# Performance work log

Hardware: AMD Instinct MI355X
Metric: run time of the kernel (lower is better)

## Reference

```python
import jax, jax.numpy as jnp
import numpy as np
from jax import lax

BS, CNT, W, P, E, K, L = 32, 128, 2048, 1024, 8, 25, 2


def setup_inputs() -> dict:
    key = jax.random.key(0)
    ks = jax.random.split(key, 12)
    s = lambda k, shape, scale: jax.random.normal(k, shape, dtype=jnp.float32) * scale
    return {
        "x": s(ks[0], (BS, CNT, W), 1.0),
        "conv_w": s(ks[1], (L, E, 1, K), 0.2),
        "conv_b": s(ks[2], (L, E), 0.02),
        "wq": s(ks[3], (L, P, W), 0.02),
        "bq": s(ks[4], (L, P), 0.02),
        "wk": s(ks[5], (L, P, W), 0.02),
        "bk": s(ks[6], (L, P), 0.02),
        "wv": s(ks[7], (L, P, W), 0.02),
        "bv": s(ks[8], (L, P), 0.02),
        "wo": s(ks[9], (L, W, P), 0.02),
        "bo": s(ks[10], (L, W), 0.02),
    }


def _moe(x, w, b):
    # x: [bs, cnt, W]; w: [E, 1, K]; b: [E]
    bs, cnt, d = x.shape
    xf = x.reshape(bs * cnt, 1, d)
    pad = K // 2
    y = lax.conv_general_dilated(
        xf, w, window_strides=(1,), padding=[(pad, pad)],
        dimension_numbers=("NCH", "OIH", "NCH"))  # [bs*cnt, E, W]
    y = y + b[None, :, None]
    return y.mean(axis=1).reshape(bs, cnt, d)


def _fe(x, wq, bq, wk, bk, wv, bv, wo, bo):
    # x: [bs, cnt, W]; projections to P, FFT-domain attention, back to W
    q = jnp.einsum("bcw,pw->bcp", x, wq) + bq
    k = jnp.einsum("bcw,pw->bcp", x, wk) + bk
    v = jnp.einsum("bcw,pw->bcp", x, wv) + bv
    q_fft = jnp.fft.fft(q, axis=-1)
    k_fft = jnp.fft.fft(k, axis=-1)
    v_fft = jnp.fft.fft(v, axis=-1)
    scale = jnp.sqrt(jnp.float32(P))
    weighted = (k_fft * jnp.conj(q_fft)) / scale * v_fft
    wv_real = jnp.fft.ifft(weighted, axis=-1).real.astype(x.dtype)
    return jnp.einsum("bcp,wp->bcw", wv_real, wo) + bo


def reference(x, conv_w, conv_b, wq, bq, wk, bk, wv, bv, wo, bo):
    for l in range(L):
        x = _moe(x, conv_w[l], conv_b[l])
        x = _fe(x, wq[l], bq[l], wk[l], bk[l], wv[l], bv[l], wo[l], bo[l])
    return x
```

## Files before the change

### kernel.cpp

```cpp
#include <hip/hip_runtime.h>
#include <hip/hip_bf16.h>

#define BSZ 32
#define CNTS 128
#define WD 2048
#define PD 1024
#define ED 8
#define KSZ 25
#define LN 2
#define MROWS (BSZ*CNTS)
#define QKVN (3*PD)
#define NWL (PD*WD)

typedef _Float16 f16;
typedef __attribute__((ext_vector_type(8))) _Float16 f16x8;
typedef __attribute__((ext_vector_type(4))) float f32x4;
typedef __attribute__((ext_vector_type(2))) float f32x2;

#define PI_F 3.14159265358979323846f
#define PAD(a) ((a) + ((a) >> 5))

__global__ __launch_bounds__(256) void cvt_layer(
    const float* __restrict__ wq, const float* __restrict__ wk,
    const float* __restrict__ wv, const float* __restrict__ wo,
    f16* __restrict__ wqkv16, f16* __restrict__ wo16)
{
    const int i = (blockIdx.x * 256 + threadIdx.x) * 4;
    const float* src;
    f16* dst;
    if (i < 3*NWL) {
        dst = wqkv16 + i;
        src = (i < NWL) ? wq + i : (i < 2*NWL) ? wk + (i - NWL) : wv + (i - 2*NWL);
    } else {
        dst = wo16 + (i - 3*NWL);
        src = wo + (i - 3*NWL);
    }
    const float4 v = *(const float4*)src;
    f16 o[4];
    o[0] = (f16)v.x; o[1] = (f16)v.y; o[2] = (f16)v.z; o[3] = (f16)v.w;
    *(ushort4*)dst = *(const ushort4*)o;
}

template<typename IT>
__global__ __launch_bounds__(256) void conv_moe(
    const IT* __restrict__ xin,
    const float* __restrict__ cw,
    const float* __restrict__ cb,
    f16* __restrict__ xo)
{
    __shared__ float srow[WD];
    __shared__ float swb[KSZ];
    __shared__ float sbb;
    const int tid = threadIdx.x;
    const size_t row = blockIdx.x;
    if (tid < KSZ) {
        float s = 0.f;
        for (int e = 0; e < ED; ++e) s += cw[e*KSZ + tid];
        swb[tid] = s * (1.f/ED);
    }
    if (tid == 32) {
        float s = 0.f;
        for (int e = 0; e < ED; ++e) s += cb[e];
        sbb = s * (1.f/ED);
    }
    const IT* xr = xin + row*WD;
    if constexpr (sizeof(IT) == 2) {
        const f16x8 v = *(const f16x8*)(xr + tid*8);
        #pragma unroll
        for (int j = 0; j < 8; ++j) srow[tid*8 + j] = (float)v[j];
    } else {
        const float4 v0 = *(const float4*)(xr + tid*8);
        const float4 v1 = *(const float4*)(xr + tid*8 + 4);
        srow[tid*8+0] = v0.x; srow[tid*8+1] = v0.y; srow[tid*8+2] = v0.z; srow[tid*8+3] = v0.w;
        srow[tid*8+4] = v1.x; srow[tid*8+5] = v1.y; srow[tid*8+6] = v1.z; srow[tid*8+7] = v1.w;
    }
    __syncthreads();
    const float bb = sbb;
    float w[32];
    #pragma unroll
    for (int k = 0; k < 32; ++k) {
        const int idx = tid*8 + k - (KSZ/2);
        w[k] = (idx >= 0 && idx < WD) ? srow[idx] : 0.f;
    }
    f16 o[8];
    #pragma unroll
    for (int j = 0; j < 8; ++j) {
        float acc = bb;
        #pragma unroll
        for (int k = 0; k < KSZ; ++k) acc = fmaf(w[j+k], swb[k], acc);
        o[j] = (f16)acc;
    }
    *(f16x8*)(xo + row*WD + tid*8) = *(const f16x8*)o;
}

template<typename OT>
__global__ __launch_bounds__(256, 2) void gemm_f16(
    const f16* __restrict__ A,
    const f16* __restrict__ B,
    const float* __restrict__ c0, const float* __restrict__ c1, const float* __restrict__ c2,
    OT* __restrict__ out,
    const int K, const int N)
{
    __shared__ f16 sA[128*64];
    __shared__ f16 sB[128*64];
    const int tid  = threadIdx.x;
    const int m0   = blockIdx.x * 128;
    const int n0   = blockIdx.y * 128;
    const int lane = tid & 63;
    const int wave = tid >> 6;
    const int wm   = (wave >> 1) * 64;
    const int wn   = (wave & 1) * 64;
    const int quad = lane >> 4;
    const int r16  = lane & 15;

    f32x4 acc[4][4] = {};

    int aoff[4];
    #pragma unroll
    for (int t = 0; t < 4; ++t) {
        const int s = tid + 256*t;
        const int row = s >> 3;
        const int sc8 = ((s & 7) ^ (row & 7)) * 8;
        aoff[t] = row * K + sc8;
    }

    int aBase[4], aXor[4], bBase[4], bXor[4];
    #pragma unroll
    for (int i = 0; i < 4; ++i) {
        const int ra = wm + i*16 + r16;
        aBase[i] = ra << 3; aXor[i] = ra & 7;
        const int rb = wn + i*16 + r16;
        bBase[i] = rb << 3; bXor[i] = rb & 7;
    }

    const size_t mK = (size_t)m0 * K;
    const size_t nK = (size_t)n0 * K;

    for (int kb = 0; kb < K; kb += 64) {
        #pragma unroll
        for (int t = 0; t < 4; ++t) {
            const int s = tid + 256*t;
            __builtin_amdgcn_global_load_lds(
                (const __attribute__((address_space(1))) unsigned int*)(A + mK + aoff[t] + kb),
                (__attribute__((address_space(3))) unsigned int*)&sA[s*8], 16, 0, 0);
            __builtin_amdgcn_global_load_lds(
                (const __attribute__((address_space(1))) unsigned int*)(B + nK + aoff[t] + kb),
                (__attribute__((address_space(3))) unsigned int*)&sB[s*8], 16, 0, 0);
        }
        __syncthreads();

        #pragma unroll
        for (int ks = 0; ks < 2; ++ks) {
            const int c = ks*4 + quad;
            f16x8 af[4], bfm[4];
            #pragma unroll
            for (int i = 0; i < 4; ++i)
                af[i] = *(const f16x8*)&sA[(aBase[i] | (c ^ aXor[i])) * 8];
            #pragma unroll
            for (int j = 0; j < 4; ++j)
                bfm[j] = *(const f16x8*)&sB[(bBase[j] | (c ^ bXor[j])) * 8];
            #pragma unroll
            for (int i = 0; i < 4; ++i)
                #pragma unroll
                for (int j = 0; j < 4; ++j)
                    acc[i][j] = __builtin_amdgcn_mfma_f32_16x16x32_f16(af[i], bfm[j], acc[i][j], 0, 0, 0);
        }
        __syncthreads();
    }

    #pragma unroll
    for (int j = 0; j < 4; ++j) {
        const int col = n0 + wn + j*16 + r16;
        const float bv = (col < 1024) ? c0[col] : (col < 2048) ? c1[col-1024] : c2[col-2048];
        #pragma unroll
        for (int i = 0; i < 4; ++i) {
            #pragma unroll
            for (int r = 0; r < 4; ++r) {
                const int rowg = m0 + wm + i*16 + quad*4 + r;
                out[(size_t)rowg*N + col] = (OT)(acc[i][j][r] + bv);
            }
        }
    }
}

__global__ __launch_bounds__(512, 2) void gemm192(
    const f16* __restrict__ A,
    const f16* __restrict__ B,
    const float* __restrict__ c0, const float* __restrict__ c1, const float* __restrict__ c2,
    f16* __restrict__ out,
    const int K, const int N)
{
    __shared__ __align__(16) f16 sA[2][2][128*64];
    __shared__ __align__(16) f16 sB[2][3][64*64];

    const int tid  = threadIdx.x;
    const int lane = tid & 63;
    const int wave = tid >> 6;
    const int wr   = wave >> 2;
    const int wc   = wave & 3;
    const int quad = lane >> 4;
    const int r16  = lane & 15;
    const int xrA  = r16 & 7;

    const int orig = blockIdx.x;
    const int xcd  = orig & 7;
    const int loc  = orig >> 3;
    const int mt   = (xcd >> 1) * 4 + (loc & 3);
    const int nt   = (xcd & 1) * 8 + (loc >> 2);
    const int m0   = mt * 256;
    const int n0   = nt * 192;

    f32x4 acc[8][3] = {};
    f16x8 bf[3][2];
    f16x8 aX0, aX1, aX2, aX3, aY0, aY1, aY2, aY3, aZ0, aZ1, aZ2, aZ3;

    int soffA[2];
    #pragma unroll
    for (int t = 0; t < 2; ++t) {
        const int s = tid + 512*t;
        const int row = s >> 3;
        soffA[t] = row * K + (((s & 7) ^ (row & 7)) * 8);
    }
    int soffB;
    {
        const int row = tid >> 3;
        soffB = row * K + (((tid & 7) ^ (row & 7)) * 8);
    }

    int bPiece[3], bBase[3], bXor[3];
    #pragma unroll
    for (int j = 0; j < 3; ++j) {
        const int rb = wc*48 + j*16 + r16;
        bPiece[j] = rb >> 6;
        bBase[j]  = (rb & 63) << 3;
        bXor[j]   = rb & 7;
    }

    const f16* Abase[2] = { A + (size_t)m0 * K, A + (size_t)(m0 + 128) * K };
    const f16* Bp[3]    = { B + (size_t)n0 * K, B + (size_t)(n0 + 64) * K,
                            B + (size_t)(n0 + 128) * K };

    #define STAGE_A(BUF, HALF, GOFF)                                              \
      { _Pragma("unroll") for (int t = 0; t < 2; ++t) {                           \
          __builtin_amdgcn_global_load_lds(                                       \
            (const __attribute__((address_space(1))) unsigned int*)(Abase[HALF] + soffA[t] + (GOFF)), \
            (__attribute__((address_space(3))) unsigned int*)&sA[BUF][HALF][(tid + 512*t)*8], \
            16, 0, 0); } }

    #define STAGE_B(BUF, PIECE, GOFF)                                             \
      { __builtin_amdgcn_global_load_lds(                                         \
          (const __attribute__((address_space(1))) unsigned int*)(Bp[PIECE] + soffB + (GOFF)), \
          (__attribute__((address_space(3))) unsigned int*)&sB[BUF][PIECE][tid*8], \
          16, 0, 0); }

    #define LDA(BUF, ROW, C) \
      (*(const f16x8*)&sA[BUF][wr][ (((ROW) << 3) + ((C) ^ xrA)) * 8 ])

    #define LDB(BUF, J, C) \
      (*(const f16x8*)&sB[BUF][bPiece[J]][ (bBase[J] + ((C) ^ bXor[J])) * 8 ])

    #define READ_BF(BUF)                                                          \
      { _Pragma("unroll") for (int j = 0; j < 3; ++j) {                           \
          bf[j][0] = LDB(BUF, j, quad);                                           \
          bf[j][1] = LDB(BUF, j, 4 + quad);                                       \
        } }

    #define READ_A(BUF, Q, D0, D1, D2, D3)                                        \
      D0 = LDA(BUF, (2*(Q))*16   + r16, quad);                                    \
      D1 = LDA(BUF, (2*(Q))*16   + r16, 4 + quad);                                \
      D2 = LDA(BUF, (2*(Q)+1)*16 + r16, quad);                                    \
      D3 = LDA(BUF, (2*(Q)+1)*16 + r16, 4 + quad);

    #define MFMA_Q(Q, D0, D1, D2, D3)                                             \
      __builtin_amdgcn_s_setprio(1);                                              \
      { _Pragma("unroll") for (int jj = 0; jj < 3; ++jj) {                        \
          acc[2*(Q)][jj]   = __builtin_amdgcn_mfma_f32_16x16x32_f16(D0, bf[jj][0], acc[2*(Q)][jj],   0,0,0); \
          acc[2*(Q)+1][jj] = __builtin_amdgcn_mfma_f32_16x16x32_f16(D2, bf[jj][0], acc[2*(Q)+1][jj], 0,0,0); \
        } }                                                                       \
      { _Pragma("unroll") for (int jj = 0; jj < 3; ++jj) {                        \
          acc[2*(Q)][jj]   = __builtin_amdgcn_mfma_f32_16x16x32_f16(D1, bf[jj][1], acc[2*(Q)][jj],   0,0,0); \
          acc[2*(Q)+1][jj] = __builtin_amdgcn_mfma_f32_16x16x32_f16(D3, bf[jj][1], acc[2*(Q)+1][jj], 0,0,0); \
        } }                                                                       \
      __builtin_amdgcn_s_setprio(0);

    #define LGKM(n) asm volatile("s_waitcnt lgkmcnt(" #n ")" ::: "memory");       \
                    __builtin_amdgcn_sched_barrier(0);
    #define VMC(n)  asm volatile("s_waitcnt vmcnt(" #n ")" ::: "memory");
    #define BAR()   __builtin_amdgcn_s_barrier();

    STAGE_B(0, 0, 0); STAGE_B(0, 1, 0); STAGE_B(0, 2, 0);
    STAGE_A(0, 0, 0); STAGE_A(0, 1, 0);
    STAGE_B(1, 0, 64); STAGE_B(1, 1, 64); STAGE_B(1, 2, 64);
    VMC(3)
    BAR()

    const int NIT = K >> 7;
    for (int it = 0; it < NIT; ++it) {
        const bool kl = (it == NIT - 1);
        const int kb1 = (2*it + 1) * 64;
        const int kb2 = kb1 + 64;
        const int kb3 = kb1 + 128;

        STAGE_A(1, 0, kb1);
        READ_BF(0)
        READ_A(0, 0, aX0, aX1, aX2, aX3)
        LGKM(0)
        MFMA_Q(0, aX0, aX1, aX2, aX3)
        BAR()
        STAGE_A(1, 1, kb1);
        READ_A(0, 1, aY0, aY1, aY2, aY3)
        READ_A(0, 2, aZ0, aZ1, aZ2, aZ3)
        LGKM(4)
        MFMA_Q(1, aY0, aY1, aY2, aY3)
        if (!kl) { STAGE_B(0, 0, kb2); STAGE_B(0, 1, kb2); }
        READ_A(0, 3, aX0, aX1, aX2, aX3)
        LGKM(4)
        MFMA_Q(2, aZ0, aZ1, aZ2, aZ3)
        if (!kl) { STAGE_B(0, 2, kb2); }
        LGKM(0)
        MFMA_Q(3, aX0, aX1, aX2, aX3)
        if (!kl) { VMC(3) } else { VMC(0) }
        BAR()

        if (!kl) STAGE_A(0, 0, kb2);
        READ_BF(1)
        READ_A(1, 0, aX0, aX1, aX2, aX3)
        LGKM(0)
        MFMA_Q(0, aX0, aX1, aX2, aX3)
        BAR()
        if (!kl) STAGE_A(0, 1, kb2);
        READ_A(1, 1, aY0, aY1, aY2, aY3)
        READ_A(1, 2, aZ0, aZ1, aZ2, aZ3)
        LGKM(4)
        MFMA_Q(1, aY0, aY1, aY2, aY3)
        if (!kl) { STAGE_B(1, 0, kb3); STAGE_B(1, 1, kb3); }
        READ_A(1, 3, aX0, aX1, aX2, aX3)
        LGKM(4)
        MFMA_Q(2, aZ0, aZ1, aZ2, aZ3)
        if (!kl) { STAGE_B(1, 2, kb3); }
        LGKM(0)
        MFMA_Q(3, aX0, aX1, aX2, aX3)
        if (!kl) { VMC(3) }
        BAR()
    }

    #pragma unroll
    for (int j = 0; j < 3; ++j) {
        const int col = n0 + wc*48 + j*16 + r16;
        const float bv = (col < 1024) ? c0[col] : (col < 2048) ? c1[col-1024] : c2[col-2048];
        #pragma unroll
        for (int mi = 0; mi < 8; ++mi) {
            #pragma unroll
            for (int r = 0; r < 4; ++r) {
                const int rowg = m0 + wr*128 + mi*16 + quad*4 + r;
                out[(size_t)rowg*N + col] = (f16)(acc[mi][j][r] + bv);
            }
        }
    }

    #undef STAGE_A
    #undef STAGE_B
    #undef LDA
    #undef LDB
    #undef READ_BF
    #undef READ_A
    #undef MFMA_Q
    #undef LGKM
    #undef VMC
    #undef BAR
}

__device__ inline void fft1024r4(f32x2* x, f32x2* y, const int tid,
                                 const float* tws, const float* twc)
{
    f32x2* src = x;
    f32x2* dst = y;
    #pragma unroll
    for (int st = 0; st < 5; ++st) {
        const int ls = 2*st;
        const int s  = 1 << ls;
        const int p  = tid >> ls;
        const int q  = tid & (s - 1);
        const f32x2 a = src[PAD(tid)];
        const f32x2 b = src[PAD(tid + 256)];
        const f32x2 c = src[PAD(tid + 512)];
        const f32x2 d = src[PAD(tid + 768)];
        const float ws = tws[st], wc = twc[st];
        const float apcx = a.x + c.x, apcy = a.y + c.y;
        const float amcx = a.x - c.x, amcy = a.y - c.y;
        const float bpdx = b.x + d.x, bpdy = b.y + d.y;
        const float bmdx = b.x - d.x, bmdy = b.y - d.y;
        f32x2 y0; y0.x = apcx + bpdx; y0.y = apcy + bpdy;
        const float t1x = amcx + bmdy, t1y = amcy - bmdx;
        const float t2x = apcx - bpdx, t2y = apcy - bpdy;
        const float t3x = amcx - bmdy, t3y = amcy + bmdx;
        const float w2x = wc*wc - ws*ws, w2y = 2.f*wc*ws;
        const float w3x = w2x*wc - w2y*ws, w3y = w2x*ws + w2y*wc;
        f32x2 y1; y1.x = wc*t1x - ws*t1y;   y1.y = wc*t1y + ws*t1x;
        f32x2 y2; y2.x = w2x*t2x - w2y*t2y; y2.y = w2x*t2y + w2y*t2x;
        f32x2 y3; y3.x = w3x*t3x - w3y*t3y; y3.y = w3x*t3y + w3y*t3x;
        const int base = q + ((p * s) << 2);
        dst[PAD(base)]       = y0;
        dst[PAD(base + s)]   = y1;
        dst[PAD(base + 2*s)] = y2;
        dst[PAD(base + 3*s)] = y3;
        __syncthreads();
        f32x2* t = src; src = dst; dst = t;
    }
}

__global__ __launch_bounds__(256) void fft_attn2(
    const f16* __restrict__ qkv, f16* __restrict__ outg)
{
    __shared__ f32x2 X[PAD(1023)+1], Y[PAD(1023)+1];
    __shared__ f16 st[2*QKVN];
    const int tid = threadIdx.x;
    const size_t row0 = (size_t)blockIdx.x * 2;
    const f16* r1 = qkv + row0*QKVN;
    const f16* r2 = r1 + QKVN;

    #pragma unroll
    for (int p = 0; p < 3; ++p) {
        const int c = tid + 256*p;
        const f16* src = (c < 384) ? (r1 + (c)*8) : (r2 + (c - 384)*8);
        *(f16x8*)&st[c*8] = *(const f16x8*)src;
    }

    float tws[5], twc[5];
    #pragma unroll
    for (int s5 = 0; s5 < 5; ++s5) {
        const int ls = 2*s5;
        const int p  = tid >> ls;
        __sincosf(-2.f*PI_F * (float)p / (float)(1024 >> ls), &tws[s5], &twc[s5]);
    }
    __syncthreads();

    const f16* s1 = st;
    const f16* s2 = st + QKVN;

    f32x2 V1[4], V2[4], S1[4], S2[4];

    #pragma unroll
    for (int k = 0; k < 4; ++k) {
        const int i = tid + 256*k;
        f32x2 t; t.x = (float)s1[2048+i]; t.y = (float)s2[2048+i];
        X[PAD(i)] = t;
    }
    __syncthreads();
    fft1024r4(X, Y, tid, tws, twc);
    #pragma unroll
    for (int k = 0; k < 4; ++k) {
        const int f = tid + 256*k;
        const int g = (PD - f) & (PD-1);
        const f32x2 z1 = Y[PAD(f)], z2 = Y[PAD(g)];
        V1[k].x = 0.5f*(z1.x + z2.x); V1[k].y = 0.5f*(z1.y - z2.y);
        V2[k].x = 0.5f*(z1.y + z2.y); V2[k].y = 0.5f*(z2.x - z1.x);
    }

    #pragma unroll
    for (int k = 0; k < 4; ++k) {
        const int i = tid + 256*k;
        f32x2 t; t.x = (float)s1[i]; t.y = (float)s1[1024+i];
        X[PAD(i)] = t;
    }
    __syncthreads();
    fft1024r4(X, Y, tid, tws, twc);
    #pragma unroll
    for (int k = 0; k < 4; ++k) {
        const int f = tid + 256*k;
        const int g = (PD - f) & (PD-1);
        const f32x2 z1 = Y[PAD(f)], z2 = Y[PAD(g)];
        const float Qr = 0.5f*(z1.x + z2.x), Qi = 0.5f*(z1.y - z2.y);
        const float Kr = 0.5f*(z1.y + z2.y), Ki = 0.5f*(z2.x - z1.x);
        const float Pr = (Kr*Qr + Ki*Qi) * (1.f/32.f);
        const float Pi = (Ki*Qr - Kr*Qi) * (1.f/32.f);
        S1[k].x = Pr*V1[k].x - Pi*V1[k].y;
        S1[k].y = -(Pr*V1[k].y + Pi*V1[k].x);
    }

    #pragma unroll
    for (int k = 0; k < 4; ++k) {
        const int i = tid + 256*k;
        f32x2 t; t.x = (float)s2[i]; t.y = (float)s2[1024+i];
        X[PAD(i)] = t;
    }
    __syncthreads();
    fft1024r4(X, Y, tid, tws, twc);
    #pragma unroll
    for (int k = 0; k < 4; ++k) {
        const int f = tid + 256*k;
        const int g = (PD - f) & (PD-1);
        const f32x2 z1 = Y[PAD(f)], z2 = Y[PAD(g)];
        const float Qr = 0.5f*(z1.x + z2.x), Qi = 0.5f*(z1.y - z2.y);
        const float Kr = 0.5f*(z1.y + z2.y), Ki = 0.5f*(z2.x - z1.x);
        const float Pr = (Kr*Qr + Ki*Qi) * (1.f/32.f);
        const float Pi = (Ki*Qr - Kr*Qi) * (1.f/32.f);
        S2[k].x = Pr*V2[k].x - Pi*V2[k].y;
        S2[k].y = -(Pr*V2[k].y + Pi*V2[k].x);
    }

    #pragma unroll
    for (int k = 0; k < 4; ++k) {
        const int f = tid + 256*k;
        f32x2 t; t.x = S1[k].x - S2[k].y; t.y = S1[k].y + S2[k].x;
        X[PAD(f)] = t;
    }
    __syncthreads();
    fft1024r4(X, Y, tid, tws, twc);
    f16* o1 = outg + row0*PD;
    f16* o2 = o1 + PD;
    #pragma unroll
    for (int k = 0; k < 4; ++k) {
        const int n = tid + 256*k;
        const f32x2 z = Y[PAD(n)];
        o1[n] = (f16)(z.x * (1.f/1024.f));
        o2[n] = (f16)(z.y * (1.f/1024.f));
    }
}

extern "C" void kernel_launch(void* const* d_in, const int* in_sizes, int n_in,
                              void* d_out, int out_size, void* d_ws, size_t ws_size,
                              hipStream_t stream)
{
    const float* x      = (const float*)d_in[0];
    const float* conv_w = (const float*)d_in[1];
    const float* conv_b = (const float*)d_in[2];
    const float* wq     = (const float*)d_in[3];
    const float* bq     = (const float*)d_in[4];
    const float* wk     = (const float*)d_in[5];
    const float* bk     = (const float*)d_in[6];
    const float* wv     = (const float*)d_in[7];
    const float* bv     = (const float*)d_in[8];
    const float* wo     = (const float*)d_in[9];
    const float* bo     = (const float*)d_in[10];

    char* ws = (char*)d_ws;
    const size_t MB = 1024*1024;
    f16*   wqkv16 = (f16*)(ws);
    f16*   wo16   = (f16*)(ws + 12*MB);
    f16*   qkvbuf = (f16*)(ws + 16*MB);
    f16*   xc16   = (f16*)(ws + 40*MB);
    f16*   xmid   = (f16*)(ws + 56*MB);
    f16*   wvr16  = xc16;

    for (int l = 0; l < LN; ++l) {
        cvt_layer<<<dim3(4*NWL/4/256), dim3(256), 0, stream>>>(
            wq + (size_t)l*NWL, wk + (size_t)l*NWL, wv + (size_t)l*NWL, wo + (size_t)l*NWL,
            wqkv16, wo16);

        if (l == 0)
            conv_moe<float><<<dim3(MROWS), dim3(256), 0, stream>>>(
                x, conv_w, conv_b, xc16);
        else
            conv_moe<f16><<<dim3(MROWS), dim3(256), 0, stream>>>(
                xmid, conv_w + (size_t)l*ED*KSZ, conv_b + (size_t)l*ED, xc16);

        gemm192<<<dim3((MROWS/256)*(QKVN/192)), dim3(512), 0, stream>>>(
            xc16, wqkv16,
            bq + (size_t)l*PD, bk + (size_t)l*PD, bv + (size_t)l*PD,
            qkvbuf, WD, QKVN);

        fft_attn2<<<dim3(MROWS/2), dim3(256), 0, stream>>>(qkvbuf, wvr16);

        if (l == LN-1)
            gemm_f16<float><<<dim3(MROWS/128, WD/128), dim3(256), 0, stream>>>(
                wvr16, wo16,
                bo + (size_t)l*WD, bo + (size_t)l*WD + PD, bo + (size_t)l*WD + PD,
                (float*)d_out, PD, WD);
        else
            gemm_f16<f16><<<dim3(MROWS/128, WD/128), dim3(256), 0, stream>>>(
                wvr16, wo16,
                bo + (size_t)l*WD, bo + (size_t)l*WD + PD, bo + (size_t)l*WD + PD,
                xmid, PD, WD);
    }
}
```

Before: 404.0 us.

## Replace output-projection GEMM with double-buffered 256x128 pipelined kernel with XCD tile mapping

Replaces the simple single-buffered 128x128 output-projection GEMM with a 512-thread kernel using 256x128 tiles. It double-buffers A and B in LDS, interleaves staged global-to-LDS loads with MFMA quarters under explicit waitcnt, barrier and setprio control, and remaps block IDs so each XCD works on a contiguous group of tiles. The aim is to hide memory latency and improve L2 reuse in the wo projection, copying the scheme already used for the QKV GEMM. In exchange the grid has fewer blocks, 256 in total, and the hand-scheduled pipeline adds complexity and the risk of subtle sync errors.

```diff
diff --git a/kernel.cpp b/kernel.cpp
--- a/kernel.cpp
+++ b/kernel.cpp
@@ -93,96 +93,6 @@
     *(f16x8*)(xo + row*WD + tid*8) = *(const f16x8*)o;
 }
 
-template<typename OT>
-__global__ __launch_bounds__(256, 2) void gemm_f16(
-    const f16* __restrict__ A,
-    const f16* __restrict__ B,
-    const float* __restrict__ c0, const float* __restrict__ c1, const float* __restrict__ c2,
-    OT* __restrict__ out,
-    const int K, const int N)
-{
-    __shared__ f16 sA[128*64];
-    __shared__ f16 sB[128*64];
-    const int tid  = threadIdx.x;
-    const int m0   = blockIdx.x * 128;
-    const int n0   = blockIdx.y * 128;
-    const int lane = tid & 63;
-    const int wave = tid >> 6;
-    const int wm   = (wave >> 1) * 64;
-    const int wn   = (wave & 1) * 64;
-    const int quad = lane >> 4;
-    const int r16  = lane & 15;
-
-    f32x4 acc[4][4] = {};
-
-    int aoff[4];
-    #pragma unroll
-    for (int t = 0; t < 4; ++t) {
-        const int s = tid + 256*t;
-        const int row = s >> 3;
-        const int sc8 = ((s & 7) ^ (row & 7)) * 8;
-        aoff[t] = row * K + sc8;
-    }
-
-    int aBase[4], aXor[4], bBase[4], bXor[4];
-    #pragma unroll
-    for (int i = 0; i < 4; ++i) {
-        const int ra = wm + i*16 + r16;
-        aBase[i] = ra << 3; aXor[i] = ra & 7;
-        const int rb = wn + i*16 + r16;
-        bBase[i] = rb << 3; bXor[i] = rb & 7;
-    }
-
-    const size_t mK = (size_t)m0 * K;
-    const size_t nK = (size_t)n0 * K;
-
-    for (int kb = 0; kb < K; kb += 64) {
-        #pragma unroll
-        for (int t = 0; t < 4; ++t) {
-            const int s = tid + 256*t;
-            __builtin_amdgcn_global_load_lds(
-                (const __attribute__((address_space(1))) unsigned int*)(A + mK + aoff[t] + kb),
-                (__attribute__((address_space(3))) unsigned int*)&sA[s*8], 16, 0, 0);
-            __builtin_amdgcn_global_load_lds(
-                (const __attribute__((address_space(1))) unsigned int*)(B + nK + aoff[t] + kb),
-                (__attribute__((address_space(3))) unsigned int*)&sB[s*8], 16, 0, 0);
-        }
-        __syncthreads();
-
-        #pragma unroll
-        for (int ks = 0; ks < 2; ++ks) {
-            const int c = ks*4 + quad;
-            f16x8 af[4], bfm[4];
-            #pragma unroll
-            for (int i = 0; i < 4; ++i)
-                af[i] = *(const f16x8*)&sA[(aBase[i] | (c ^ aXor[i])) * 8];
-            #pragma unroll
-            for (int j = 0; j < 4; ++j)
-                bfm[j] = *(const f16x8*)&sB[(bBase[j] | (c ^ bXor[j])) * 8];
-            #pragma unroll
-            for (int i = 0; i < 4; ++i)
-                #pragma unroll
-                for (int j = 0; j < 4; ++j)
-                    acc[i][j] = __builtin_amdgcn_mfma_f32_16x16x32_f16(af[i], bfm[j], acc[i][j], 0, 0, 0);
-        }
-        __syncthreads();
-    }
-
-    #pragma unroll
-    for (int j = 0; j < 4; ++j) {
-        const int col = n0 + wn + j*16 + r16;
-        const float bv = (col < 1024) ? c0[col] : (col < 2048) ? c1[col-1024] : c2[col-2048];
-        #pragma unroll
-        for (int i = 0; i < 4; ++i) {
-            #pragma unroll
-            for (int r = 0; r < 4; ++r) {
-                const int rowg = m0 + wm + i*16 + quad*4 + r;
-                out[(size_t)rowg*N + col] = (OT)(acc[i][j][r] + bv);
-            }
-        }
-    }
-}
-
 __global__ __launch_bounds__(512, 2) void gemm192(
     const f16* __restrict__ A,
     const f16* __restrict__ B,
@@ -354,6 +264,193 @@
             for (int r = 0; r < 4; ++r) {
                 const int rowg = m0 + wr*128 + mi*16 + quad*4 + r;
                 out[(size_t)rowg*N + col] = (f16)(acc[mi][j][r] + bv);
+            }
+        }
+    }
+
+    #undef STAGE_A
+    #undef STAGE_B
+    #undef LDA
+    #undef LDB
+    #undef READ_BF
+    #undef READ_A
+    #undef MFMA_Q
+    #undef LGKM
+    #undef VMC
+    #undef BAR
+}
+
+template<typename OT>
+__global__ __launch_bounds__(512, 2) void gemmOP(
+    const f16* __restrict__ A,
+    const f16* __restrict__ B,
+    const float* __restrict__ c0, const float* __restrict__ c1,
+    OT* __restrict__ out,
+    const int K, const int N)
+{
+    __shared__ __align__(16) f16 sA[2][2][128*64];
+    __shared__ __align__(16) f16 sB[2][2][64*64];
+
+    const int tid  = threadIdx.x;
+    const int lane = tid & 63;
+    const int wave = tid >> 6;
+    const int wr   = wave >> 2;
+    const int wc   = wave & 3;
+    const int quad = lane >> 4;
+    const int r16  = lane & 15;
+    const int xrA  = r16 & 7;
+
+    const int orig = blockIdx.x;
+    const int xcd  = orig & 7;
+    const int loc  = orig >> 3;
+    const int mt   = (xcd >> 1) * 4 + (loc & 3);
+    const int nt   = (xcd & 1) * 8 + (loc >> 2);
+    const int m0   = mt * 256;
+    const int n0   = nt * 128;
+
+    f32x4 acc[8][2] = {};
+    f16x8 bf[2][2];
+    f16x8 aX0, aX1, aX2, aX3, aY0, aY1, aY2, aY3, aZ0, aZ1, aZ2, aZ3;
+
+    int soffA[2];
+    #pragma unroll
+    for (int t = 0; t < 2; ++t) {
+        const int s = tid + 512*t;
+        const int row = s >> 3;
+        soffA[t] = row * K + (((s & 7) ^ (row & 7)) * 8);
+    }
+    int soffB;
+    {
+        const int row = tid >> 3;
+        soffB = row * K + (((tid & 7) ^ (row & 7)) * 8);
+    }
+
+    int bPiece[2], bBase[2], bXor[2];
+    #pragma unroll
+    for (int j = 0; j < 2; ++j) {
+        const int rb = wc*32 + j*16 + r16;
+        bPiece[j] = rb >> 6;
+        bBase[j]  = (rb & 63) << 3;
+        bXor[j]   = rb & 7;
+    }
+
+    const f16* Abase[2] = { A + (size_t)m0 * K, A + (size_t)(m0 + 128) * K };
+    const f16* Bp[2]    = { B + (size_t)n0 * K, B + (size_t)(n0 + 64) * K };
+
+    #define STAGE_A(BUF, HALF, GOFF)                                              \
+      { _Pragma("unroll") for (int t = 0; t < 2; ++t) {                           \
+          __builtin_amdgcn_global_load_lds(                                       \
+            (const __attribute__((address_space(1))) unsigned int*)(Abase[HALF] + soffA[t] + (GOFF)), \
+            (__attribute__((address_space(3))) unsigned int*)&sA[BUF][HALF][(tid + 512*t)*8], \
+            16, 0, 0); } }
+
+    #define STAGE_B(BUF, PIECE, GOFF)                                             \
+      { __builtin_amdgcn_global_load_lds(                                         \
+          (const __attribute__((address_space(1))) unsigned int*)(Bp[PIECE] + soffB + (GOFF)), \
+          (__attribute__((address_space(3))) unsigned int*)&sB[BUF][PIECE][tid*8], \
+          16, 0, 0); }
+
+    #define LDA(BUF, ROW, C) \
+      (*(const f16x8*)&sA[BUF][wr][ (((ROW) << 3) + ((C) ^ xrA)) * 8 ])
+
+    #define LDB(BUF, J, C) \
+      (*(const f16x8*)&sB[BUF][bPiece[J]][ (bBase[J] + ((C) ^ bXor[J])) * 8 ])
+
+    #define READ_BF(BUF)                                                          \
+      { _Pragma("unroll") for (int j = 0; j < 2; ++j) {                           \
+          bf[j][0] = LDB(BUF, j, quad);                                           \
+          bf[j][1] = LDB(BUF, j, 4 + quad);                                       \
+        } }
+
+    #define READ_A(BUF, Q, D0, D1, D2, D3)                                        \
+      D0 = LDA(BUF, (2*(Q))*16   + r16, quad);                                    \
+      D1 = LDA(BUF, (2*(Q))*16   + r16, 4 + quad);                                \
+      D2 = LDA(BUF, (2*(Q)+1)*16 + r16, quad);                                    \
+      D3 = LDA(BUF, (2*(Q)+1)*16 + r16, 4 + quad);
+
+    #define MFMA_Q(Q, D0, D1, D2, D3)                                             \
+      __builtin_amdgcn_s_setprio(1);                                              \
+      { _Pragma("unroll") for (int jj = 0; jj < 2; ++jj) {                        \
+          acc[2*(Q)][jj]   = __builtin_amdgcn_mfma_f32_16x16x32_f16(D0, bf[jj][0], acc[2*(Q)][jj],   0,0,0); \
+          acc[2*(Q)+1][jj] = __builtin_amdgcn_mfma_f32_16x16x32_f16(D2, bf[jj][0], acc[2*(Q)+1][jj], 0,0,0); \
+        } }                                                                       \
+      { _Pragma("unroll") for (int jj = 0; jj < 2; ++jj) {                        \
+          acc[2*(Q)][jj]   = __builtin_amdgcn_mfma_f32_16x16x32_f16(D1, bf[jj][1], acc[2*(Q)][jj],   0,0,0); \
+          acc[2*(Q)+1][jj] = __builtin_amdgcn_mfma_f32_16x16x32_f16(D3, bf[jj][1], acc[2*(Q)+1][jj], 0,0,0); \
+        } }                                                                       \
+      __builtin_amdgcn_s_setprio(0);
+
+    #define LGKM(n) asm volatile("s_waitcnt lgkmcnt(" #n ")" ::: "memory");       \
+                    __builtin_amdgcn_sched_barrier(0);
+    #define VMC(n)  asm volatile("s_waitcnt vmcnt(" #n ")" ::: "memory");
+    #define BAR()   __builtin_amdgcn_s_barrier();
+
+    STAGE_B(0, 0, 0); STAGE_B(0, 1, 0);
+    STAGE_A(0, 0, 0); STAGE_A(0, 1, 0);
+    STAGE_B(1, 0, 64); STAGE_B(1, 1, 64);
+    VMC(2)
+    BAR()
+
+    const int NIT = K >> 7;
+    for (int it = 0; it < NIT; ++it) {
+        const bool kl = (it == NIT - 1);
+        const int kb1 = (2*it + 1) * 64;
+        const int kb2 = kb1 + 64;
+        const int kb3 = kb1 + 128;
+
+        STAGE_A(1, 0, kb1);
+        READ_BF(0)
+        READ_A(0, 0, aX0, aX1, aX2, aX3)
+        LGKM(0)
+        MFMA_Q(0, aX0, aX1, aX2, aX3)
+        BAR()
+        STAGE_A(1, 1, kb1);
+        READ_A(0, 1, aY0, aY1, aY2, aY3)
+        READ_A(0, 2, aZ0, aZ1, aZ2, aZ3)
+        LGKM(4)
+        MFMA_Q(1, aY0, aY1, aY2, aY3)
+        if (!kl) { STAGE_B(0, 0, kb2); }
+        READ_A(0, 3, aX0, aX1, aX2, aX3)
+        LGKM(4)
+        MFMA_Q(2, aZ0, aZ1, aZ2, aZ3)
+        if (!kl) { STAGE_B(0, 1, kb2); }
+        LGKM(0)
+        MFMA_Q(3, aX0, aX1, aX2, aX3)
+        if (!kl) { VMC(2) } else { VMC(0) }
+        BAR()
+
+        if (!kl) STAGE_A(0, 0, kb2);
+        READ_BF(1)
+        READ_A(1, 0, aX0, aX1, aX2, aX3)
+        LGKM(0)
+        MFMA_Q(0, aX0, aX1, aX2, aX3)
+        BAR()
+        if (!kl) STAGE_A(0, 1, kb2);
+        READ_A(1, 1, aY0, aY1, aY2, aY3)
+        READ_A(1, 2, aZ0, aZ1, aZ2, aZ3)
+        LGKM(4)
+        MFMA_Q(1, aY0, aY1, aY2, aY3)
+        if (!kl) { STAGE_B(1, 0, kb3); }
+        READ_A(1, 3, aX0, aX1, aX2, aX3)
+        LGKM(4)
+        MFMA_Q(2, aZ0, aZ1, aZ2, aZ3)
+        if (!kl) { STAGE_B(1, 1, kb3); }
+        LGKM(0)
+        MFMA_Q(3, aX0, aX1, aX2, aX3)
+        if (!kl) { VMC(2) }
+        BAR()
+    }
+
+    #pragma unroll
+    for (int j = 0; j < 2; ++j) {
+        const int col = n0 + wc*32 + j*16 + r16;
+        const float bv = (col < 1024) ? c0[col] : c1[col-1024];
+        #pragma unroll
+        for (int mi = 0; mi < 8; ++mi) {
+            #pragma unroll
+            for (int r = 0; r < 4; ++r) {
+                const int rowg = m0 + wr*128 + mi*16 + quad*4 + r;
+                out[(size_t)rowg*N + col] = (OT)(acc[mi][j][r] + bv);
             }
         }
     }
@@ -563,14 +660,14 @@
         fft_attn2<<<dim3(MROWS/2), dim3(256), 0, stream>>>(qkvbuf, wvr16);
 
         if (l == LN-1)
-            gemm_f16<float><<<dim3(MROWS/128, WD/128), dim3(256), 0, stream>>>(
+            gemmOP<float><<<dim3((MROWS/256)*(WD/128)), dim3(512), 0, stream>>>(
                 wvr16, wo16,
-                bo + (size_t)l*WD, bo + (size_t)l*WD + PD, bo + (size_t)l*WD + PD,
+                bo + (size_t)l*WD, bo + (size_t)l*WD + PD,
                 (float*)d_out, PD, WD);
         else
-            gemm_f16<f16><<<dim3(MROWS/128, WD/128), dim3(256), 0, stream>>>(
+            gemmOP<f16><<<dim3((MROWS/256)*(WD/128)), dim3(512), 0, stream>>>(
                 wvr16, wo16,
-                bo + (size_t)l*WD, bo + (size_t)l*WD + PD, bo + (size_t)l*WD + PD,
+                bo + (size_t)l*WD, bo + (size_t)l*WD + PD,
                 xmid, PD, WD);
     }
 }
```

Result: no change. 411.9 us (+2.0%).
